# Performance work log

Hardware: AMD Instinct MI355X
Metric: run time of the kernel (lower is better)

## Reference

```python
import jax, jax.numpy as jnp
import numpy as np

HIDDEN = 2048
N_HEADS = 16
N_KV_HEADS = 4
HEAD_DIM = 128
N_REP = N_HEADS // N_KV_HEADS
BATCH = 2
SEQ = 2048
SCALE = HEAD_DIM ** -0.5
NEG = -1e9


def apply_rope(x, freqs):
    # x: (b, s, h, d); freqs: (s, d//2) angles. Interleaved-pair rotation.
    cos = jnp.cos(freqs)[None, :, None, :]
    sin = jnp.sin(freqs)[None, :, None, :]
    x1 = x[..., 0::2]
    x2 = x[..., 1::2]
    r1 = x1 * cos - x2 * sin
    r2 = x1 * sin + x2 * cos
    return jnp.stack([r1, r2], axis=-1).reshape(x.shape)


def setup_inputs() -> dict:
    key = jax.random.key(0)
    ks = jax.random.split(key, 6)
    x = jax.random.normal(ks[0], (BATCH, SEQ, HIDDEN), dtype=jnp.float32)
    wq = jax.random.normal(ks[1], (N_HEADS * HEAD_DIM, HIDDEN), dtype=jnp.float32) * 0.02
    wk = jax.random.normal(ks[2], (N_KV_HEADS * HEAD_DIM, HIDDEN), dtype=jnp.float32) * 0.02
    wv = jax.random.normal(ks[3], (N_KV_HEADS * HEAD_DIM, HIDDEN), dtype=jnp.float32) * 0.02
    wo = jax.random.normal(ks[4], (HIDDEN, N_HEADS * HEAD_DIM), dtype=jnp.float32) * 0.02
    # RoPE angle table: pos * theta^{-2i/d}
    inv_freq = 1.0 / (10000.0 ** (jnp.arange(0, HEAD_DIM, 2, dtype=jnp.float32) / HEAD_DIM))
    rope_freqs = jnp.arange(SEQ, dtype=jnp.float32)[:, None] * inv_freq[None, :]  # (S, d/2)
    # additive causal mask
    causal = jnp.tril(jnp.ones((SEQ, SEQ), dtype=bool))
    mask = jnp.where(causal, 0.0, NEG).astype(jnp.float32)[None, None]  # (1,1,S,S)
    return {"x": x, "wq": wq, "wk": wk, "wv": wv, "wo": wo,
            "rope_freqs": rope_freqs, "mask": mask}


def reference(x, wq, wk, wv, wo, rope_freqs, mask):
    b, s, _ = x.shape
    q = (x @ wq.T).reshape(b, s, N_HEADS, HEAD_DIM)
    k = (x @ wk.T).reshape(b, s, N_KV_HEADS, HEAD_DIM)
    v = (x @ wv.T).reshape(b, s, N_KV_HEADS, HEAD_DIM)
    q = apply_rope(q, rope_freqs)
    k = apply_rope(k, rope_freqs)
    new_k, new_v = k, v  # kv cache (no prior cache, start_pos=0)
    # GQA: repeat each kv head n_rep times (matches expand+reshape in source)
    k_rep = jnp.repeat(k, N_REP, axis=2)  # (b, s, n_heads, d)
    v_rep = jnp.repeat(v, N_REP, axis=2)
    scores = jnp.einsum('bqhd,bkhd->bhqk', q, k_rep) * SCALE
    scores = scores + mask
    attn = jax.nn.softmax(scores.astype(jnp.float32), axis=-1).astype(q.dtype)
    out = jnp.einsum('bhqk,bkhd->bqhd', attn, v_rep).reshape(b, s, -1)
    return out @ wo.T, (new_k, new_v)
```

## Files before the change

### kernel.cpp

```cpp
#include <hip/hip_runtime.h>
#include <hip/hip_bf16.h>

#define NH 16
#define NKV 4
#define HD 128
#define QSCALE 0.1275174272f

using bf16x8 = __attribute__((ext_vector_type(8))) __bf16;
using f32x4  = __attribute__((ext_vector_type(4))) float;
using u16x8  = __attribute__((ext_vector_type(8))) unsigned short;
using u16x2  = __attribute__((ext_vector_type(2))) unsigned short;

__device__ __forceinline__ unsigned short f2b(float f) {
  __hip_bfloat16 h = __float2bfloat16(f);
  return __builtin_bit_cast(unsigned short, h);
}
__device__ __forceinline__ float b2f(unsigned short u) {
  unsigned int v = ((unsigned int)u) << 16;
  return __builtin_bit_cast(float, v);
}

__device__ __forceinline__ void glds16(const unsigned short* g, unsigned short* l) {
  __builtin_amdgcn_global_load_lds(
      (const __attribute__((address_space(1))) unsigned int*)(const void*)g,
      (__attribute__((address_space(3))) unsigned int*)(void*)l, 16, 0, 0);
}

__global__ __launch_bounds__(256) void cvt_fused(const float* __restrict__ x,
                                                 const float* __restrict__ wq,
                                                 const float* __restrict__ wk,
                                                 const float* __restrict__ wv,
                                                 const float* __restrict__ wo,
                                                 unsigned short* __restrict__ xb,
                                                 unsigned short* __restrict__ wqkvb,
                                                 unsigned short* __restrict__ wob) {
  int i = blockIdx.x * 256 + threadIdx.x;
  const float* src;
  unsigned short* dst;
  int off;
  if (i < 1048576)      { src = x;  dst = xb;              off = i; }
  else if (i < 1572864) { src = wq; dst = wqkvb;           off = i - 1048576; }
  else if (i < 1703936) { src = wk; dst = wqkvb + 4194304; off = i - 1572864; }
  else if (i < 1835008) { src = wv; dst = wqkvb + 5242880; off = i - 1703936; }
  else                  { src = wo; dst = wob;             off = i - 1835008; }
  const float4* s4 = reinterpret_cast<const float4*>(src) + (size_t)off * 2;
  float4 v0 = s4[0], v1 = s4[1];
  u16x8 o;
  o[0] = f2b(v0.x); o[1] = f2b(v0.y); o[2] = f2b(v0.z); o[3] = f2b(v0.w);
  o[4] = f2b(v1.x); o[5] = f2b(v1.y); o[6] = f2b(v1.z); o[7] = f2b(v1.w);
  reinterpret_cast<u16x8*>(dst)[off] = o;
}

template<int CF32>
__global__ __launch_bounds__(256) void gemm_lds(const unsigned short* __restrict__ A,
                                                const unsigned short* __restrict__ B,
                                                void* __restrict__ C,
                                                int M, int N, int K) {
  __shared__ unsigned short As[4096];
  __shared__ unsigned short Bs[4096];
  const int tid = threadIdx.x;
  const int lane = tid & 63;
  const int wid = tid >> 6;
  const int wm = wid >> 1, wn = wid & 1;
  const int row0 = blockIdx.y * 128, col0 = blockIdx.x * 128;
  const int fr = lane & 15;
  const int fk = (lane >> 4) * 8;
  const int srow = tid >> 2;
  const int scol = (tid & 3) * 8;
  const unsigned short* Ag = A + (size_t)(row0 + srow) * K + scol;
  const unsigned short* Bg = B + (size_t)(col0 + srow) * K + scol;
  unsigned short* AsW = &As[wid * 512];
  unsigned short* BsW = &Bs[wid * 512];

  f32x4 acc[4][4];
#pragma unroll
  for (int i = 0; i < 4; i++)
#pragma unroll
    for (int j = 0; j < 4; j++) acc[i][j] = f32x4{0.f, 0.f, 0.f, 0.f};

  for (int k0 = 0; k0 < K; k0 += 32) {
    __syncthreads();
    glds16(Ag + k0,                  AsW);
    glds16(Ag + k0 + (size_t)64 * K, AsW + 2048);
    glds16(Bg + k0,                  BsW);
    glds16(Bg + k0 + (size_t)64 * K, BsW + 2048);
    __syncthreads();
    bf16x8 af[4], bfr[4];
#pragma unroll
    for (int i = 0; i < 4; i++)
      af[i] = *reinterpret_cast<const bf16x8*>(&As[(wm * 64 + i * 16 + fr) * 32 + fk]);
#pragma unroll
    for (int i = 0; i < 4; i++)
      bfr[i] = *reinterpret_cast<const bf16x8*>(&Bs[(wn * 64 + i * 16 + fr) * 32 + fk]);
#pragma unroll
    for (int i = 0; i < 4; i++)
#pragma unroll
      for (int j = 0; j < 4; j++)
        acc[i][j] = __builtin_amdgcn_mfma_f32_16x16x32_bf16(af[i], bfr[j], acc[i][j], 0, 0, 0);
  }

  const int r4 = (lane >> 4) * 4;
#pragma unroll
  for (int i = 0; i < 4; i++) {
#pragma unroll
    for (int j = 0; j < 4; j++) {
      int rb = row0 + wm * 64 + i * 16 + r4;
      int cb = col0 + wn * 64 + j * 16 + fr;
#pragma unroll
      for (int r = 0; r < 4; r++) {
        if (CF32)
          reinterpret_cast<float*>(C)[(size_t)(rb + r) * N + cb] = acc[i][j][r];
        else
          reinterpret_cast<unsigned short*>(C)[(size_t)(rb + r) * N + cb] = f2b(acc[i][j][r]);
      }
    }
  }
}

__global__ __launch_bounds__(256) void rope_kernel(const unsigned short* __restrict__ qkv,
                                                   const float* __restrict__ freqs,
                                                   unsigned short* __restrict__ qro,
                                                   unsigned short* __restrict__ kro,
                                                   float* __restrict__ newk) {
  const int NQ = 4096 * 16 * 64;
  const int NK = 4096 * 4 * 64;
  int idx = blockIdx.x * 256 + threadIdx.x;
  if (idx >= NQ + NK) return;
  if (idx < NQ) {
    int i = idx & 63;
    int h = (idx >> 6) & 15;
    int row = idx >> 10;
    int s = row & 2047, b = row >> 11;
    float f = freqs[s * 64 + i];
    float c = cosf(f), sn = sinf(f);
    u16x2 xv = *reinterpret_cast<const u16x2*>(qkv + (size_t)row * 3072 + h * 128 + 2 * i);
    float x1 = b2f(xv.x), x2 = b2f(xv.y);
    float r1 = (x1 * c - x2 * sn) * QSCALE;
    float r2 = (x1 * sn + x2 * c) * QSCALE;
    u16x2 o; o.x = f2b(r1); o.y = f2b(r2);
    *reinterpret_cast<u16x2*>(qro + ((size_t)(b * 16 + h) * 2048 + s) * 128 + 2 * i) = o;
  } else {
    idx -= NQ;
    int i = idx & 63;
    int h = (idx >> 6) & 3;
    int row = idx >> 8;
    int s = row & 2047, b = row >> 11;
    float f = freqs[s * 64 + i];
    float c = cosf(f), sn = sinf(f);
    u16x2 xv = *reinterpret_cast<const u16x2*>(qkv + (size_t)row * 3072 + 2048 + h * 128 + 2 * i);
    float x1 = b2f(xv.x), x2 = b2f(xv.y);
    float r1 = x1 * c - x2 * sn;
    float r2 = x1 * sn + x2 * c;
    u16x2 o; o.x = f2b(r1); o.y = f2b(r2);
    *reinterpret_cast<u16x2*>(kro + ((size_t)(b * 4 + h) * 2048 + s) * 128 + 2 * i) = o;
    float2 of; of.x = r1; of.y = r2;
    *reinterpret_cast<float2*>(newk + (size_t)row * 512 + h * 128 + 2 * i) = of;
  }
}

__global__ __launch_bounds__(256) void vtrans_kernel(const unsigned short* __restrict__ qkv,
                                                     unsigned short* __restrict__ vt,
                                                     float* __restrict__ newv) {
  __shared__ unsigned short T[32][136];
  const int st = blockIdx.x;
  const int kvh = blockIdx.y & 3, b = blockIdx.y >> 2;
  const int s0 = st * 32;
  const int t = threadIdx.x;
  const int ls = t >> 3;
  const int ch = (t & 7) * 2;
  const unsigned short* src = qkv + (size_t)(b * 2048 + s0 + ls) * 3072 + 2560 + kvh * 128 + ch * 8;
  u16x8 a0 = *reinterpret_cast<const u16x8*>(src);
  u16x8 a1 = *reinterpret_cast<const u16x8*>(src + 8);
  *reinterpret_cast<u16x8*>(&T[ls][ch * 8])     = a0;
  *reinterpret_cast<u16x8*>(&T[ls][ch * 8 + 8]) = a1;
  float* nv = newv + (size_t)(b * 2048 + s0 + ls) * 512 + kvh * 128 + ch * 8;
  float4 f0, f1, f2, f3;
  f0.x = b2f(a0[0]); f0.y = b2f(a0[1]); f0.z = b2f(a0[2]); f0.w = b2f(a0[3]);
  f1.x = b2f(a0[4]); f1.y = b2f(a0[5]); f1.z = b2f(a0[6]); f1.w = b2f(a0[7]);
  f2.x = b2f(a1[0]); f2.y = b2f(a1[1]); f2.z = b2f(a1[2]); f2.w = b2f(a1[3]);
  f3.x = b2f(a1[4]); f3.y = b2f(a1[5]); f3.z = b2f(a1[6]); f3.w = b2f(a1[7]);
  reinterpret_cast<float4*>(nv)[0] = f0;
  reinterpret_cast<float4*>(nv)[1] = f1;
  reinterpret_cast<float4*>(nv)[2] = f2;
  reinterpret_cast<float4*>(nv)[3] = f3;
  __syncthreads();
  const int d = t >> 1, half = t & 1;
  unsigned short* dst = vt + ((size_t)(b * 4 + kvh) * 128 + d) * 2048 + s0 + half * 16;
  u16x8 o0, o1;
#pragma unroll
  for (int q = 0; q < 8; q++) {
    int slot = half * 16 + q;
    int kl = ((slot >> 2) & 1) * 16 + (slot >> 3) * 4 + (slot & 3);
    o0[q] = T[kl][d];
  }
#pragma unroll
  for (int q = 0; q < 8; q++) {
    int slot = half * 16 + 8 + q;
    int kl = ((slot >> 2) & 1) * 16 + (slot >> 3) * 4 + (slot & 3);
    o1[q] = T[kl][d];
  }
  reinterpret_cast<u16x8*>(dst)[0] = o0;
  reinterpret_cast<u16x8*>(dst)[1] = o1;
}

__global__ __launch_bounds__(256, 4) void attn_kernel(const unsigned short* __restrict__ qro,
                                                      const unsigned short* __restrict__ kro,
                                                      const unsigned short* __restrict__ vt,
                                                      unsigned short* __restrict__ out) {
  __shared__ unsigned short Ks[2][32 * 128];
  __shared__ unsigned short Vs[2][64 * 64];
  const int tid = threadIdx.x, lane = tid & 63, w = tid >> 6;
  const int kvhb = blockIdx.x & 7;
  const int kvh = kvhb & 3, b = kvhb >> 2;
  const int t = 127 - (blockIdx.x >> 3);
  const int h = kvh * 4 + w;
  const int qbase = t * 16;
  const int fr = lane & 15, g = lane >> 4, fk = g * 8;
  const unsigned short* Kp = kro + (size_t)(b * 4 + kvh) * 2048 * 128;
  const unsigned short* Vtp = vt + (size_t)(b * 4 + kvh) * 128 * 2048;
  const unsigned short* Qp = qro + ((size_t)(b * 16 + h) * 2048 + qbase) * 128;

  bf16x8 qf[4];
#pragma unroll
  for (int kk = 0; kk < 4; kk++)
    qf[kk] = *reinterpret_cast<const bf16x8*>(Qp + fr * 128 + kk * 32 + fk);

  u16x8 onesu;
#pragma unroll
  for (int j = 0; j < 8; j++) onesu[j] = 0x3F80;
  bf16x8 ones = __builtin_bit_cast(bf16x8, onesu);

  f32x4 o[8];
#pragma unroll
  for (int dt = 0; dt < 8; dt++) o[dt] = f32x4{0.f, 0.f, 0.f, 0.f};
  f32x4 dacc = f32x4{0.f, 0.f, 0.f, 0.f};
  const int qrow_s = qbase + fr;
  const int nfull = (qbase >= 31) ? ((qbase - 31) >> 5) + 1 : 0;
  const int niter = nfull + 1;

  const int krow = w * 8 + (lane >> 4);
  const int kcol = lane & 15;
  const int vrow = w * 16 + (lane >> 3);
  const int vcol = lane & 7;

  auto stage = [&](int kv0, int buf) {
    unsigned short* Kb = &Ks[buf][0];
    unsigned short* Vb = &Vs[buf][0];
#pragma unroll
    for (int j = 0; j < 2; j++) {
      int r = krow + j * 4;
      glds16(Kp + (size_t)(kv0 + r) * 128 + ((kcol ^ (r & 7)) * 8),
             Kb + (w * 8 + j * 4) * 128);
    }
#pragma unroll
    for (int j = 0; j < 2; j++) {
      int r = vrow + j * 8;
      int u = vcol ^ (r & 7);
      int d = 2 * r + (u >> 2);
      glds16(Vtp + (size_t)d * 2048 + kv0 + (u & 3) * 8,
             Vb + (w * 16 + j * 8) * 64);
    }
  };

  auto step = [&](int kv0, bool mask, int buf) {
    const unsigned short* Kb = &Ks[buf][0];
    const unsigned short* Vb = &Vs[buf][0];
    f32x4 sc[2];
    sc[0] = sc[1] = f32x4{0.f, 0.f, 0.f, 0.f};
    __builtin_amdgcn_s_setprio(1);
#pragma unroll
    for (int kk = 0; kk < 4; kk++) {
      int blk = ((kk * 4 + g) ^ (fr & 7)) * 8;
      bf16x8 ka0 = *reinterpret_cast<const bf16x8*>(Kb + (fr +  0) * 128 + blk);
      bf16x8 ka1 = *reinterpret_cast<const bf16x8*>(Kb + (fr + 16) * 128 + blk);
      sc[0] = __builtin_amdgcn_mfma_f32_16x16x32_bf16(ka0, qf[kk], sc[0], 0, 0, 0);
      sc[1] = __builtin_amdgcn_mfma_f32_16x16x32_bf16(ka1, qf[kk], sc[1], 0, 0, 0);
    }
    __builtin_amdgcn_s_setprio(0);
#pragma unroll
    for (int s = 0; s < 2; s++)
#pragma unroll
      for (int r = 0; r < 4; r++) {
        float v = sc[s][r];
        if (mask && (kv0 + 16 * s + 4 * g + r > qrow_s)) v = -1e30f;
        sc[s][r] = __builtin_amdgcn_exp2f(v);
      }
    u16x8 pau;
#pragma unroll
    for (int j = 0; j < 4; j++) {
      pau[j]     = f2b(sc[0][j]);
      pau[4 + j] = f2b(sc[1][j]);
    }
    bf16x8 pa = __builtin_bit_cast(bf16x8, pau);
    dacc = __builtin_amdgcn_mfma_f32_16x16x32_bf16(pa, ones, dacc, 0, 0, 0);
    __builtin_amdgcn_s_setprio(1);
#pragma unroll
    for (int dt = 0; dt < 8; dt++) {
      int jr = dt * 8 + (fr >> 1);
      int c = ((fr & 1) * 4 + g) ^ (fr >> 1);
      bf16x8 vf = *reinterpret_cast<const bf16x8*>(Vb + jr * 64 + c * 8);
      o[dt] = __builtin_amdgcn_mfma_f32_16x16x32_bf16(pa, vf, o[dt], 0, 0, 0);
    }
    __builtin_amdgcn_s_setprio(0);
  };

  stage(0, 0);
  int buf = 0;
  for (int i = 0; i < niter; i++) {
    __syncthreads();
    if (i + 1 < niter) stage((i + 1) * 32, buf ^ 1);
    step(i * 32, i == nfull, buf);
    buf ^= 1;
  }

#pragma unroll
  for (int r = 0; r < 4; r++) {
    float inv = 1.0f / dacc[r];
    int qrow = qbase + g * 4 + r;
    size_t rowoff = ((size_t)b * 2048 + qrow) * 2048 + (size_t)h * 128;
#pragma unroll
    for (int dt = 0; dt < 8; dt++)
      out[rowoff + dt * 16 + fr] = f2b(o[dt][r] * inv);
  }
}

extern "C" void kernel_launch(void* const* d_in, const int* in_sizes, int n_in,
                              void* d_out, int out_size, void* d_ws, size_t ws_size,
                              hipStream_t stream) {
  const float* x  = (const float*)d_in[0];
  const float* wq = (const float*)d_in[1];
  const float* wk = (const float*)d_in[2];
  const float* wv = (const float*)d_in[3];
  const float* wo = (const float*)d_in[4];
  const float* freqs = (const float*)d_in[5];

  char* ws = (char*)d_ws;
  unsigned short* xb    = (unsigned short*)(ws);
  unsigned short* attn  = xb;
  unsigned short* wqkvb = (unsigned short*)(ws + 16777216);
  unsigned short* wob   = (unsigned short*)(ws + 29360128);
  unsigned short* qkv   = (unsigned short*)(ws + 37748736);
  unsigned short* qro   = (unsigned short*)(ws + 62914560);
  unsigned short* kro   = (unsigned short*)(ws + 79691776);
  unsigned short* vt    = (unsigned short*)(ws + 83886080);

  float* out_o = (float*)d_out;
  float* out_k = (float*)d_out + 8388608;
  float* out_v = (float*)d_out + 10485760;

  cvt_fused<<<9216, 256, 0, stream>>>(x, wq, wk, wv, wo, xb, wqkvb, wob);

  gemm_lds<0><<<dim3(24, 32), 256, 0, stream>>>(xb, wqkvb, qkv, 4096, 3072, 2048);

  rope_kernel<<<20480, 256, 0, stream>>>(qkv, freqs, qro, kro, out_k);
  vtrans_kernel<<<dim3(64, 8), 256, 0, stream>>>(qkv, vt, out_v);

  attn_kernel<<<1024, 256, 0, stream>>>(qro, kro, vt, attn);

  gemm_lds<1><<<dim3(16, 32), 256, 0, stream>>>(attn, wob, out_o, 4096, 2048, 2048);
}
```

Measured before the change: 224.5 us.

## Replace GEMM with 256x128 tiles, multi-buffered async LDS loads and swizzle

Both projection GEMMs now use a new kernel with 256x128 output tiles per block. A tiles are triple-buffered and B tiles double-buffered in LDS, loaded asynchronously with vmcnt-based waits so global loads overlap the MFMA work. The LDS layout uses an XOR swizzle to avoid bank conflicts, and s_setprio raises priority around the MFMA block. Each block keeps more accumulators in registers, and there are half as many blocks (384 and 256), which could hurt occupancy or wave balance on the device.

Result: slower. 242.6 us (+8.1%).

```diff
diff --git a/kernel.cpp b/kernel.cpp
--- a/kernel.cpp
+++ b/kernel.cpp
@@ -52,59 +52,102 @@
 }
 
 template<int CF32>
-__global__ __launch_bounds__(256) void gemm_lds(const unsigned short* __restrict__ A,
-                                                const unsigned short* __restrict__ B,
-                                                void* __restrict__ C,
-                                                int M, int N, int K) {
-  __shared__ unsigned short As[4096];
-  __shared__ unsigned short Bs[4096];
-  const int tid = threadIdx.x;
-  const int lane = tid & 63;
-  const int wid = tid >> 6;
+__global__ __launch_bounds__(256, 2) void gemm_big(const unsigned short* __restrict__ A,
+                                                   const unsigned short* __restrict__ B,
+                                                   void* __restrict__ C,
+                                                   int N, int K) {
+  __shared__ unsigned short As[3][8192];
+  __shared__ unsigned short Bs[2][4096];
+  const int tid = threadIdx.x, lane = tid & 63, wid = tid >> 6;
   const int wm = wid >> 1, wn = wid & 1;
-  const int row0 = blockIdx.y * 128, col0 = blockIdx.x * 128;
-  const int fr = lane & 15;
-  const int fk = (lane >> 4) * 8;
-  const int srow = tid >> 2;
-  const int scol = (tid & 3) * 8;
-  const unsigned short* Ag = A + (size_t)(row0 + srow) * K + scol;
-  const unsigned short* Bg = B + (size_t)(col0 + srow) * K + scol;
-  unsigned short* AsW = &As[wid * 512];
-  unsigned short* BsW = &Bs[wid * 512];
-
-  f32x4 acc[4][4];
-#pragma unroll
-  for (int i = 0; i < 4; i++)
+  const int row0 = blockIdx.y * 256, col0 = blockIdx.x * 128;
+  const int fr = lane & 15, g = lane >> 4;
+  const int NT = K >> 5;
+
+  size_t offA[4], offB[2];
+#pragma unroll
+  for (int l = 0; l < 4; l++) {
+    int cid = tid + l * 256;
+    int R = cid >> 3, cp = cid & 7;
+    int cl = cp ^ (R & 7);
+    offA[l] = (size_t)(row0 + 2 * R + (cl >> 2)) * K + (cl & 3) * 8;
+  }
+#pragma unroll
+  for (int l = 0; l < 2; l++) {
+    int cid = tid + l * 256;
+    int R = cid >> 3, cp = cid & 7;
+    int cl = cp ^ (R & 7);
+    offB[l] = (size_t)(col0 + 2 * R + (cl >> 2)) * K + (cl & 3) * 8;
+  }
+
+  auto stageA = [&](int t, int sb) {
+    int k0 = t * 32;
+#pragma unroll
+    for (int l = 0; l < 4; l++)
+      glds16(A + offA[l] + k0, &As[sb][tid * 8 + l * 2048]);
+  };
+  auto stageB = [&](int t, int sb) {
+    int k0 = t * 32;
+#pragma unroll
+    for (int l = 0; l < 2; l++)
+      glds16(B + offB[l] + k0, &Bs[sb][tid * 8 + l * 2048]);
+  };
+
+  f32x4 acc[8][4];
+#pragma unroll
+  for (int i = 0; i < 8; i++)
 #pragma unroll
     for (int j = 0; j < 4; j++) acc[i][j] = f32x4{0.f, 0.f, 0.f, 0.f};
 
-  for (int k0 = 0; k0 < K; k0 += 32) {
-    __syncthreads();
-    glds16(Ag + k0,                  AsW);
-    glds16(Ag + k0 + (size_t)64 * K, AsW + 2048);
-    glds16(Bg + k0,                  BsW);
-    glds16(Bg + k0 + (size_t)64 * K, BsW + 2048);
-    __syncthreads();
-    bf16x8 af[4], bfr[4];
-#pragma unroll
-    for (int i = 0; i < 4; i++)
-      af[i] = *reinterpret_cast<const bf16x8*>(&As[(wm * 64 + i * 16 + fr) * 32 + fk]);
-#pragma unroll
-    for (int i = 0; i < 4; i++)
-      bfr[i] = *reinterpret_cast<const bf16x8*>(&Bs[(wn * 64 + i * 16 + fr) * 32 + fk]);
-#pragma unroll
-    for (int i = 0; i < 4; i++)
+  stageA(0, 0);
+  stageB(0, 0);
+  stageA(1, 1);
+  asm volatile("s_waitcnt vmcnt(4)" ::: "memory");
+  __builtin_amdgcn_s_barrier();
+  asm volatile("" ::: "memory");
+
+  const int cp8 = ((((fr & 1) << 2) | g) ^ ((fr >> 1) & 7)) * 8;
+  const int rrA = (fr >> 1);
+
+  int rbA = 0, sbA = 2, rbB = 0;
+#pragma unroll 1
+  for (int t = 0; t < NT; ++t) {
+    if (t + 1 < NT) stageB(t + 1, rbB ^ 1);
+    if (t + 2 < NT) stageA(t + 2, sbA);
+
+    bf16x8 af[8], bfr[4];
+#pragma unroll
+    for (int i = 0; i < 8; i++)
+      af[i] = *reinterpret_cast<const bf16x8*>(&As[rbA][(wm * 64 + i * 8 + rrA) * 64 + cp8]);
+#pragma unroll
+    for (int j = 0; j < 4; j++)
+      bfr[j] = *reinterpret_cast<const bf16x8*>(&Bs[rbB][(wn * 32 + j * 8 + rrA) * 64 + cp8]);
+
+    __builtin_amdgcn_s_setprio(1);
+#pragma unroll
+    for (int i = 0; i < 8; i++)
 #pragma unroll
       for (int j = 0; j < 4; j++)
         acc[i][j] = __builtin_amdgcn_mfma_f32_16x16x32_bf16(af[i], bfr[j], acc[i][j], 0, 0, 0);
-  }
-
-  const int r4 = (lane >> 4) * 4;
-#pragma unroll
-  for (int i = 0; i < 4; i++) {
+    __builtin_amdgcn_s_setprio(0);
+
+    if (t + 1 < NT) {
+      if (t + 2 < NT) asm volatile("s_waitcnt vmcnt(4)" ::: "memory");
+      else            asm volatile("s_waitcnt vmcnt(0)" ::: "memory");
+      __builtin_amdgcn_s_barrier();
+      asm volatile("" ::: "memory");
+    }
+    rbA = rbA == 2 ? 0 : rbA + 1;
+    sbA = sbA == 2 ? 0 : sbA + 1;
+    rbB ^= 1;
+  }
+
+  const int r4 = g * 4;
+#pragma unroll
+  for (int i = 0; i < 8; i++) {
 #pragma unroll
     for (int j = 0; j < 4; j++) {
-      int rb = row0 + wm * 64 + i * 16 + r4;
+      int rb = row0 + wm * 128 + i * 16 + r4;
       int cb = col0 + wn * 64 + j * 16 + fr;
 #pragma unroll
       for (int r = 0; r < 4; r++) {
@@ -350,12 +393,12 @@
 
   cvt_fused<<<9216, 256, 0, stream>>>(x, wq, wk, wv, wo, xb, wqkvb, wob);
 
-  gemm_lds<0><<<dim3(24, 32), 256, 0, stream>>>(xb, wqkvb, qkv, 4096, 3072, 2048);
+  gemm_big<0><<<dim3(24, 16), 256, 0, stream>>>(xb, wqkvb, qkv, 3072, 2048);
 
   rope_kernel<<<20480, 256, 0, stream>>>(qkv, freqs, qro, kro, out_k);
   vtrans_kernel<<<dim3(64, 8), 256, 0, stream>>>(qkv, vt, out_v);
 
   attn_kernel<<<1024, 256, 0, stream>>>(qro, kro, vt, attn);
 
-  gemm_lds<1><<<dim3(16, 32), 256, 0, stream>>>(attn, wob, out_o, 4096, 2048, 2048);
-}
+  gemm_big<1><<<dim3(16, 16), 256, 0, stream>>>(attn, wob, out_o, 2048, 2048);
+}
```
